# Kernel tuning notes

Hardware: AMD Instinct MI355X
Metric: run time of the kernel (lower is better)

## Reference

```python
import jax, jax.numpy as jnp
import numpy as np

SUB_NO = 20
E_NO = 2000
I_NO = 500
T_NO = 200
M_NO = 8
B_NO = 12
T_DATA = 50000


def _binary_tree_cden(sub_no):
    C = np.zeros((sub_no, sub_no), np.float32)
    for p in range(sub_no):
        for c in (2 * p + 1, 2 * p + 2):
            if c < sub_no:
                C[p, c] = 1.0
    return jnp.asarray(C)


def _syn_assign(n_syn, sub_no):
    # one-hot synapse -> subunit assignment, [sub_no, n_syn]
    return jax.nn.one_hot(jnp.arange(n_syn) % sub_no, sub_no, dtype=jnp.float32).T


def setup_inputs() -> dict:
    key = jax.random.key(0)
    ks = jax.random.split(key, 12)
    S_e = jax.random.uniform(ks[0], (T_DATA, E_NO), jnp.float32)
    S_i = jax.random.uniform(ks[1], (T_DATA, I_NO), jnp.float32)
    # parameters (scaled randn so tanh/exp stay in a sane range)
    conv1_e_bases = jax.random.normal(ks[2], (B_NO, T_NO), jnp.float32)
    conv1_e_weights = 0.001 * jax.random.normal(ks[3], (M_NO * SUB_NO, B_NO), jnp.float32)
    conv1_i_bases = jax.random.normal(ks[4], (B_NO, T_NO), jnp.float32)
    conv1_i_weights = 0.001 * jax.random.normal(ks[5], (M_NO * SUB_NO, B_NO), jnp.float32)
    conv2_bases = jax.random.normal(ks[6], (B_NO, T_NO), jnp.float32)
    conv2_weights = 0.05 * jax.random.normal(ks[7], (M_NO * SUB_NO, B_NO), jnp.float32)
    leaf_linear = 0.3 * jax.random.normal(ks[8], (SUB_NO, M_NO), jnp.float32)
    multiplex_linear = 0.3 * jax.random.normal(ks[9], (SUB_NO, M_NO), jnp.float32)
    multiplex_bias = 0.3 * jax.random.normal(ks[10], (SUB_NO,), jnp.float32)
    return {
        "S_e": S_e, "S_i": S_i,
        "C_den": _binary_tree_cden(SUB_NO),
        "C_syn_e": _syn_assign(E_NO, SUB_NO),
        "C_syn_i": _syn_assign(I_NO, SUB_NO),
        "conv1_e_bases": conv1_e_bases, "conv1_e_weights": conv1_e_weights,
        "conv1_i_bases": conv1_i_bases, "conv1_i_weights": conv1_i_weights,
        "conv2_bases": conv2_bases, "conv2_weights": conv2_weights,
        "leaf_linear": leaf_linear, "multiplex_linear": multiplex_linear,
        "multiplex_bias": multiplex_bias,
    }


def _causal_conv1d(x, w, groups):
    # x: [1, C_in, T], w: [C_out, C_in/groups, K]; left-pad K-1 -> causal
    K = w.shape[-1]
    return jax.lax.conv_general_dilated(
        x, w, window_strides=(1,), padding=[(K - 1, 0)],
        feature_group_count=groups)


def reference(S_e, S_i, C_den, C_syn_e, C_syn_i,
              conv1_e_bases, conv1_e_weights, conv1_i_bases, conv1_i_weights,
              conv2_bases, conv2_weights, leaf_linear, multiplex_linear,
              multiplex_bias):
    T = S_e.shape[0]
    sub_no, M = multiplex_linear.shape
    # route synapses to subunits: [1, sub_no, T]
    Se = (S_e @ C_syn_e.T).T[None]
    Si = (S_i @ C_syn_i.T).T[None]
    # low-rank kernels: [M*sub_no, 1, T_no]
    k1e = (conv1_e_weights @ conv1_e_bases)[:, None, :]
    k1i = (conv1_i_weights @ conv1_i_bases)[:, None, :]
    k2 = (conv2_weights @ conv2_bases)[:, None, :]
    # grouped causal conv (groups = sub_no, M outputs per group)
    e1 = _causal_conv1d(Se, k1e, sub_no)[0].T.reshape(T, sub_no, M)
    i1 = _causal_conv1d(Si, k1i, sub_no)[0].T.reshape(T, sub_no, M)
    S_conv = e1 + i1  # [T, sub_no, M]
    expL = jnp.exp(leaf_linear)      # [sub_no, M]
    expM = jnp.exp(multiplex_linear)  # [sub_no, M]
    sub_out = jnp.zeros((T, sub_no), S_e.dtype)
    # reverse order: children (larger indices) computed before parents;
    # masked matmul == torch's gather of leaf children (zeros where C_den[p]==0)
    for p in range(sub_no - 1, -1, -1):
        leaf_in = (sub_out * C_den[p][None, :]) @ expL  # [T, M]
        h = jnp.tanh(S_conv[:, p, :] + leaf_in)         # [T, M]
        c2 = _causal_conv1d(h.T[None], k2[p * M:(p + 1) * M], M)[0].T  # depthwise
        g = jnp.tanh(c2)
        sub_out = sub_out.at[:, p].set(g @ expM[p] + multiplex_bias[p])
    return sub_out[:, 0]
```

## Files before the change

kernel.cpp:

```cpp
#include <hip/hip_runtime.h>
#include <math.h>

#define T_DATA 50000
#define E_NO   2000
#define I_NO   500
#define SUBN   20
#define MN     8
#define KLEN   200
#define TILE   512
#define HALO   199
#define TW     712

__device__ __forceinline__ void conv4(float acc[4], const float4 L,
                                      const float4 H, const float4 k4) {
  const float w0 = L.x, w1 = L.y, w2 = L.z, w3 = L.w;
  const float w4 = H.x, w5 = H.y, w6 = H.z;
  acc[0] += k4.x * w3; acc[1] += k4.x * w4; acc[2] += k4.x * w5; acc[3] += k4.x * w6;
  acc[0] += k4.y * w2; acc[1] += k4.y * w3; acc[2] += k4.y * w4; acc[3] += k4.y * w5;
  acc[0] += k4.z * w1; acc[1] += k4.z * w2; acc[2] += k4.z * w3; acc[3] += k4.z * w4;
  acc[0] += k4.w * w0; acc[1] += k4.w * w1; acc[2] += k4.w * w2; acc[3] += k4.w * w3;
}

__global__ __launch_bounds__(256) void precompute_k(
    const float* __restrict__ we, const float* __restrict__ be,
    const float* __restrict__ wi, const float* __restrict__ bi,
    const float* __restrict__ w2, const float* __restrict__ b2,
    float* __restrict__ k1e, float* __restrict__ k1i, float* __restrict__ k2) {
  int idx = blockIdx.x * 256 + threadIdx.x;
  if (idx >= 160 * KLEN) return;
  int row = idx / KLEN, d = idx % KLEN;
  int col = KLEN - 1 - d;
  float se = 0.f, si = 0.f, s2 = 0.f;
#pragma unroll
  for (int b = 0; b < 12; ++b) {
    se += we[row * 12 + b] * be[b * KLEN + col];
    si += wi[row * 12 + b] * bi[b * KLEN + col];
    s2 += w2[row * 12 + b] * b2[b * KLEN + col];
  }
  k1e[idx] = se; k1i[idx] = si; k2[idx] = s2;
}

__global__ __launch_bounds__(320) void route_kernel(
    const float* __restrict__ S_e, const float* __restrict__ S_i,
    float* __restrict__ Se, float* __restrict__ Si) {
  __shared__ float lds_e[1280];
  __shared__ float lds_i[500];
  int tid = threadIdx.x;
  int t0 = blockIdx.x * 4;
  for (int tt = 0; tt < 4; ++tt) {
    int t = t0 + tt;
    const float4* rowE = (const float4*)(S_e + (size_t)t * E_NO);
    float4 a = rowE[tid];
    if (tid < 180) {
      float4 b = rowE[tid + 320];
      a.x += b.x; a.y += b.y; a.z += b.z; a.w += b.w;
    }
    ((float4*)lds_e)[tid] = a;
    if (tid < 125) {
      const float4* rowI = (const float4*)(S_i + (size_t)t * I_NO);
      ((float4*)lds_i)[tid] = rowI[tid];
    }
    __syncthreads();
    if (tid < 20) {
      float s = 0.f;
#pragma unroll
      for (int k = 0; k < 64; ++k) s += lds_e[tid + 20 * k];
      Se[tid * T_DATA + t] = s;
    } else if (tid >= 64 && tid < 84) {
      int r = tid - 64;
      float s = 0.f;
#pragma unroll
      for (int k = 0; k < 25; ++k) s += lds_i[r + 20 * k];
      Si[r * T_DATA + t] = s;
    }
    __syncthreads();
  }
}

__global__ __launch_bounds__(256) void conv1_kernel(
    const float* __restrict__ Se, const float* __restrict__ Si,
    const float* __restrict__ k1e, const float* __restrict__ k1i,
    float* __restrict__ Sconv) {
  __shared__ float xe_raw[TW + 4], xi_raw[TW + 4];
  __shared__ float ke[MN * KLEN], ki[MN * KLEN];
  float* xe = xe_raw + 4;
  float* xi = xi_raw + 4;
  int s = blockIdx.y;
  int t0 = blockIdx.x * TILE;
  int tid = threadIdx.x;

  for (int idx = tid; idx < TW; idx += 256) {
    int t = t0 - HALO + idx;
    bool ok = (t >= 0) && (t < T_DATA) && (idx < 711);
    xe[idx] = ok ? Se[s * T_DATA + t] : 0.f;
    xi[idx] = ok ? Si[s * T_DATA + t] : 0.f;
  }
  for (int idx = tid; idx < MN * KLEN; idx += 256) {
    ke[idx] = k1e[s * MN * KLEN + idx];
    ki[idx] = k1i[s * MN * KLEN + idx];
  }
  __syncthreads();

  int m = tid >> 5, g = tid & 31;
  const float* kem = ke + m * KLEN;
  const float* kim = ki + m * KLEN;
  float* outp = Sconv + ((size_t)(s * MN + m)) * T_DATA + t0;

#pragma unroll 1
  for (int i = 0; i < 4; ++i) {
    const int U = 4 * g + 128 * i;
    const int S0 = U + 196;
    float4 Le = *(const float4*)(xe + S0);
    float4 He = *(const float4*)(xe + S0 + 4);
    float4 Lx = *(const float4*)(xi + S0);
    float4 Hx = *(const float4*)(xi + S0 + 4);
    float acc[4] = {0.f, 0.f, 0.f, 0.f};
    for (int d0 = 0; d0 < KLEN; d0 += 8) {
      float4 ka = *(const float4*)(kem + d0);
      float4 kb = *(const float4*)(kim + d0);
      conv4(acc, Le, He, ka);
      conv4(acc, Lx, Hx, kb);
      float4 Ne = *(const float4*)(xe + S0 - d0 - 4);
      float4 Nx = *(const float4*)(xi + S0 - d0 - 4);
      ka = *(const float4*)(kem + d0 + 4);
      kb = *(const float4*)(kim + d0 + 4);
      conv4(acc, Ne, Le, ka);
      conv4(acc, Nx, Lx, kb);
      He = Ne; Le = *(const float4*)(xe + S0 - d0 - 8);
      Hx = Nx; Lx = *(const float4*)(xi + S0 - d0 - 8);
    }
    if (t0 + U < T_DATA)
      *(float4*)(outp + U) = make_float4(acc[0], acc[1], acc[2], acc[3]);
  }
}

struct LevelArgs {
  int node[8];
  int c1[8];
  int c2[8];
};

__global__ __launch_bounds__(256) void level_kernel(
    const float* __restrict__ Sconv, const float* __restrict__ k2r,
    const float* __restrict__ leaf_lin, const float* __restrict__ mult_lin,
    const float* __restrict__ mult_bias, float* __restrict__ sub_out,
    float* __restrict__ d_out, LevelArgs args) {
  __shared__ float hbuf_raw[4 + MN * TW];
  __shared__ float k2l[MN * KLEN];
  __shared__ float red[MN * TILE];
  float* hbuf = hbuf_raw + 4;
  int tid = threadIdx.x;
  int t0 = blockIdx.x * TILE;
  int ni = blockIdx.y;
  int p = args.node[ni], c1 = args.c1[ni], c2 = args.c2[ni];

  for (int idx = tid; idx < MN * KLEN; idx += 256)
    k2l[idx] = k2r[p * MN * KLEN + idx];

  for (int m = 0; m < MN; ++m) {
    float eL1 = (c1 >= 0) ? expf(leaf_lin[c1 * MN + m]) : 0.f;
    float eL2 = (c2 >= 0) ? expf(leaf_lin[c2 * MN + m]) : 0.f;
    const float* scp = Sconv + ((size_t)(p * MN + m)) * T_DATA;
    const float* s1 = sub_out + (size_t)((c1 >= 0) ? c1 : 0) * T_DATA;
    const float* s2 = sub_out + (size_t)((c2 >= 0) ? c2 : 0) * T_DATA;
    for (int idx = tid; idx < TW; idx += 256) {
      int t = t0 - HALO + idx;
      float v = 0.f;
      if (t >= 0 && t < T_DATA && idx < 711) {
        float x = scp[t];
        if (c1 >= 0) x += eL1 * s1[t];
        if (c2 >= 0) x += eL2 * s2[t];
        v = tanhf(x);
      }
      hbuf[m * TW + idx] = v;
    }
  }
  __syncthreads();

  int m = tid >> 5, g = tid & 31;
  const float* km = k2l + m * KLEN;
  const float* hm = hbuf + m * TW;
  float eM = expf(mult_lin[p * MN + m]);

#pragma unroll 1
  for (int i = 0; i < 4; ++i) {
    const int U = 4 * g + 128 * i;
    const int S0 = U + 196;
    float4 L = *(const float4*)(hm + S0);
    float4 H = *(const float4*)(hm + S0 + 4);
    float acc[4] = {0.f, 0.f, 0.f, 0.f};
    for (int d0 = 0; d0 < KLEN; d0 += 8) {
      float4 ka = *(const float4*)(km + d0);
      conv4(acc, L, H, ka);
      float4 N = *(const float4*)(hm + S0 - d0 - 4);
      ka = *(const float4*)(km + d0 + 4);
      conv4(acc, N, L, ka);
      H = N; L = *(const float4*)(hm + S0 - d0 - 8);
    }
    *(float4*)(red + m * TILE + U) =
        make_float4(tanhf(acc[0]) * eM, tanhf(acc[1]) * eM,
                    tanhf(acc[2]) * eM, tanhf(acc[3]) * eM);
  }
  __syncthreads();

  float bias = mult_bias[p];
  float* outp = (p == 0) ? d_out : (sub_out + (size_t)p * T_DATA);
  for (int k = 0; k < 2; ++k) {
    int tl2 = tid + k * 256;
    int t = t0 + tl2;
    if (t < T_DATA) {
      float ssum = bias;
#pragma unroll
      for (int mm = 0; mm < MN; ++mm) ssum += red[mm * TILE + tl2];
      outp[t] = ssum;
    }
  }
}

extern "C" void kernel_launch(void* const* d_in, const int* in_sizes, int n_in,
                              void* d_out, int out_size, void* d_ws, size_t ws_size,
                              hipStream_t stream) {
  const float* S_e  = (const float*)d_in[0];
  const float* S_i  = (const float*)d_in[1];
  const float* c1eb = (const float*)d_in[5];
  const float* c1ew = (const float*)d_in[6];
  const float* c1ib = (const float*)d_in[7];
  const float* c1iw = (const float*)d_in[8];
  const float* c2b  = (const float*)d_in[9];
  const float* c2w  = (const float*)d_in[10];
  const float* ll   = (const float*)d_in[11];
  const float* ml   = (const float*)d_in[12];
  const float* mb   = (const float*)d_in[13];

  float* ws    = (float*)d_ws;
  float* Se    = ws;
  float* Si    = ws + 1000000;
  float* Sconv = ws + 2000000;
  float* subo  = ws + 10000000;
  float* k1e   = ws + 11000000;
  float* k1i   = k1e + 32000;
  float* k2    = k1i + 32000;
  float* out   = (float*)d_out;

  precompute_k<<<dim3(125), 256, 0, stream>>>(c1ew, c1eb, c1iw, c1ib, c2w, c2b,
                                              k1e, k1i, k2);
  route_kernel<<<dim3(T_DATA / 4), 320, 0, stream>>>(S_e, S_i, Se, Si);

  int ntiles = (T_DATA + TILE - 1) / TILE;
  conv1_kernel<<<dim3(ntiles, SUBN), 256, 0, stream>>>(Se, Si, k1e, k1i, Sconv);

  LevelArgs L4 = {{15, 16, 17, 18, 19, 0, 0, 0},
                  {-1, -1, -1, -1, -1, 0, 0, 0},
                  {-1, -1, -1, -1, -1, 0, 0, 0}};
  LevelArgs L3 = {{7, 8, 9, 10, 11, 12, 13, 14},
                  {15, 17, 19, -1, -1, -1, -1, -1},
                  {16, 18, -1, -1, -1, -1, -1, -1}};
  LevelArgs L2 = {{3, 4, 5, 6, 0, 0, 0, 0},
                  {7, 9, 11, 13, 0, 0, 0, 0},
                  {8, 10, 12, 14, 0, 0, 0, 0}};
  LevelArgs L1 = {{1, 2, 0, 0, 0, 0, 0, 0},
                  {3, 5, 0, 0, 0, 0, 0, 0},
                  {4, 6, 0, 0, 0, 0, 0, 0}};
  LevelArgs L0 = {{0, 0, 0, 0, 0, 0, 0, 0},
                  {1, 0, 0, 0, 0, 0, 0, 0},
                  {2, 0, 0, 0, 0, 0, 0, 0}};

  level_kernel<<<dim3(ntiles, 5), 256, 0, stream>>>(Sconv, k2, ll, ml, mb, subo, out, L4);
  level_kernel<<<dim3(ntiles, 8), 256, 0, stream>>>(Sconv, k2, ll, ml, mb, subo, out, L3);
  level_kernel<<<dim3(ntiles, 4), 256, 0, stream>>>(Sconv, k2, ll, ml, mb, subo, out, L2);
  level_kernel<<<dim3(ntiles, 2), 256, 0, stream>>>(Sconv, k2, ll, ml, mb, subo, out, L1);
  level_kernel<<<dim3(ntiles, 1), 256, 0, stream>>>(Sconv, k2, ll, ml, mb, subo, out, L0);
}
```

Baseline: 1.052 ms.

## Fuse kernel precompute into routing, use fast tanh, and shrink level tiles

```diff
diff --git a/kernel.cpp b/kernel.cpp
--- a/kernel.cpp
+++ b/kernel.cpp
@@ -11,6 +11,14 @@
 #define HALO   199
 #define TW     712
 
+__device__ __forceinline__ float fast_tanh(float x) {
+  float ax = fabsf(x);
+  float e  = __expf(-2.f * ax);
+  float r  = __builtin_amdgcn_rcpf(1.f + e);
+  float t  = fmaf(-2.f * e, r, 1.f);
+  return copysignf(t, x);
+}
+
 __device__ __forceinline__ void conv4(float acc[4], const float4 L,
                                       const float4 H, const float4 k4) {
   const float w0 = L.x, w1 = L.y, w2 = L.z, w3 = L.w;
@@ -21,32 +29,36 @@
   acc[0] += k4.w * w0; acc[1] += k4.w * w1; acc[2] += k4.w * w2; acc[3] += k4.w * w3;
 }
 
-__global__ __launch_bounds__(256) void precompute_k(
+__global__ __launch_bounds__(320) void route_kernel(
+    const float* __restrict__ S_e, const float* __restrict__ S_i,
+    float* __restrict__ Se, float* __restrict__ Si,
     const float* __restrict__ we, const float* __restrict__ be,
     const float* __restrict__ wi, const float* __restrict__ bi,
     const float* __restrict__ w2, const float* __restrict__ b2,
     float* __restrict__ k1e, float* __restrict__ k1i, float* __restrict__ k2) {
-  int idx = blockIdx.x * 256 + threadIdx.x;
-  if (idx >= 160 * KLEN) return;
-  int row = idx / KLEN, d = idx % KLEN;
-  int col = KLEN - 1 - d;
-  float se = 0.f, si = 0.f, s2 = 0.f;
-#pragma unroll
-  for (int b = 0; b < 12; ++b) {
-    se += we[row * 12 + b] * be[b * KLEN + col];
-    si += wi[row * 12 + b] * bi[b * KLEN + col];
-    s2 += w2[row * 12 + b] * b2[b * KLEN + col];
-  }
-  k1e[idx] = se; k1i[idx] = si; k2[idx] = s2;
-}
-
-__global__ __launch_bounds__(320) void route_kernel(
-    const float* __restrict__ S_e, const float* __restrict__ S_i,
-    float* __restrict__ Se, float* __restrict__ Si) {
   __shared__ float lds_e[1280];
   __shared__ float lds_i[500];
   int tid = threadIdx.x;
-  int t0 = blockIdx.x * 4;
+  int bid = blockIdx.x;
+
+  if (bid >= 12500) {
+    int idx = (bid - 12500) * 320 + tid;
+    if (idx < 160 * KLEN) {
+      int row = idx / KLEN, d = idx % KLEN;
+      int col = KLEN - 1 - d;
+      float se = 0.f, si = 0.f, s2 = 0.f;
+#pragma unroll
+      for (int b = 0; b < 12; ++b) {
+        se += we[row * 12 + b] * be[b * KLEN + col];
+        si += wi[row * 12 + b] * bi[b * KLEN + col];
+        s2 += w2[row * 12 + b] * b2[b * KLEN + col];
+      }
+      k1e[idx] = se; k1i[idx] = si; k2[idx] = s2;
+    }
+    return;
+  }
+
+  int t0 = bid * 4;
   for (int tt = 0; tt < 4; ++tt) {
     int t = t0 + tt;
     const float4* rowE = (const float4*)(S_e + (size_t)t * E_NO);
@@ -140,17 +152,19 @@
   int c2[8];
 };
 
+template <int LT>
 __global__ __launch_bounds__(256) void level_kernel(
     const float* __restrict__ Sconv, const float* __restrict__ k2r,
     const float* __restrict__ leaf_lin, const float* __restrict__ mult_lin,
     const float* __restrict__ mult_bias, float* __restrict__ sub_out,
     float* __restrict__ d_out, LevelArgs args) {
-  __shared__ float hbuf_raw[4 + MN * TW];
+  const int TWL = LT + KLEN;
+  __shared__ float hbuf_raw[4 + MN * (LT + KLEN)];
   __shared__ float k2l[MN * KLEN];
-  __shared__ float red[MN * TILE];
+  __shared__ float red[MN * LT];
   float* hbuf = hbuf_raw + 4;
   int tid = threadIdx.x;
-  int t0 = blockIdx.x * TILE;
+  int t0 = blockIdx.x * LT;
   int ni = blockIdx.y;
   int p = args.node[ni], c1 = args.c1[ni], c2 = args.c2[ni];
 
@@ -158,32 +172,32 @@
     k2l[idx] = k2r[p * MN * KLEN + idx];
 
   for (int m = 0; m < MN; ++m) {
-    float eL1 = (c1 >= 0) ? expf(leaf_lin[c1 * MN + m]) : 0.f;
-    float eL2 = (c2 >= 0) ? expf(leaf_lin[c2 * MN + m]) : 0.f;
+    float eL1 = (c1 >= 0) ? __expf(leaf_lin[c1 * MN + m]) : 0.f;
+    float eL2 = (c2 >= 0) ? __expf(leaf_lin[c2 * MN + m]) : 0.f;
     const float* scp = Sconv + ((size_t)(p * MN + m)) * T_DATA;
     const float* s1 = sub_out + (size_t)((c1 >= 0) ? c1 : 0) * T_DATA;
     const float* s2 = sub_out + (size_t)((c2 >= 0) ? c2 : 0) * T_DATA;
-    for (int idx = tid; idx < TW; idx += 256) {
+    for (int idx = tid; idx < TWL; idx += 256) {
       int t = t0 - HALO + idx;
       float v = 0.f;
-      if (t >= 0 && t < T_DATA && idx < 711) {
+      if (t >= 0 && t < T_DATA && idx < TWL - 1) {
         float x = scp[t];
         if (c1 >= 0) x += eL1 * s1[t];
         if (c2 >= 0) x += eL2 * s2[t];
-        v = tanhf(x);
+        v = fast_tanh(x);
       }
-      hbuf[m * TW + idx] = v;
+      hbuf[m * TWL + idx] = v;
     }
   }
   __syncthreads();
 
   int m = tid >> 5, g = tid & 31;
   const float* km = k2l + m * KLEN;
-  const float* hm = hbuf + m * TW;
-  float eM = expf(mult_lin[p * MN + m]);
+  const float* hm = hbuf + m * TWL;
+  float eM = __expf(mult_lin[p * MN + m]);
 
 #pragma unroll 1
-  for (int i = 0; i < 4; ++i) {
+  for (int i = 0; i < LT / 128; ++i) {
     const int U = 4 * g + 128 * i;
     const int S0 = U + 196;
     float4 L = *(const float4*)(hm + S0);
@@ -197,22 +211,25 @@
       conv4(acc, N, L, ka);
       H = N; L = *(const float4*)(hm + S0 - d0 - 8);
     }
-    *(float4*)(red + m * TILE + U) =
-        make_float4(tanhf(acc[0]) * eM, tanhf(acc[1]) * eM,
-                    tanhf(acc[2]) * eM, tanhf(acc[3]) * eM);
+    *(float4*)(red + m * LT + U) =
+        make_float4(fast_tanh(acc[0]) * eM, fast_tanh(acc[1]) * eM,
+                    fast_tanh(acc[2]) * eM, fast_tanh(acc[3]) * eM);
   }
   __syncthreads();
 
   float bias = mult_bias[p];
   float* outp = (p == 0) ? d_out : (sub_out + (size_t)p * T_DATA);
-  for (int k = 0; k < 2; ++k) {
+#pragma unroll
+  for (int k = 0; k < (LT + 255) / 256; ++k) {
     int tl2 = tid + k * 256;
-    int t = t0 + tl2;
-    if (t < T_DATA) {
-      float ssum = bias;
-#pragma unroll
-      for (int mm = 0; mm < MN; ++mm) ssum += red[mm * TILE + tl2];
-      outp[t] = ssum;
+    if (tl2 < LT) {
+      int t = t0 + tl2;
+      if (t < T_DATA) {
+        float ssum = bias;
+#pragma unroll
+        for (int mm = 0; mm < MN; ++mm) ssum += red[mm * LT + tl2];
+        outp[t] = ssum;
+      }
     }
   }
 }
@@ -242,12 +259,11 @@
   float* k2    = k1i + 32000;
   float* out   = (float*)d_out;
 
-  precompute_k<<<dim3(125), 256, 0, stream>>>(c1ew, c1eb, c1iw, c1ib, c2w, c2b,
-                                              k1e, k1i, k2);
-  route_kernel<<<dim3(T_DATA / 4), 320, 0, stream>>>(S_e, S_i, Se, Si);
-
-  int ntiles = (T_DATA + TILE - 1) / TILE;
-  conv1_kernel<<<dim3(ntiles, SUBN), 256, 0, stream>>>(Se, Si, k1e, k1i, Sconv);
+  route_kernel<<<dim3(12600), 320, 0, stream>>>(S_e, S_i, Se, Si,
+                                                c1ew, c1eb, c1iw, c1ib, c2w, c2b,
+                                                k1e, k1i, k2);
+
+  conv1_kernel<<<dim3(98, SUBN), 256, 0, stream>>>(Se, Si, k1e, k1i, Sconv);
 
   LevelArgs L4 = {{15, 16, 17, 18, 19, 0, 0, 0},
                   {-1, -1, -1, -1, -1, 0, 0, 0},
@@ -265,9 +281,9 @@
                   {1, 0, 0, 0, 0, 0, 0, 0},
                   {2, 0, 0, 0, 0, 0, 0, 0}};
 
-  level_kernel<<<dim3(ntiles, 5), 256, 0, stream>>>(Sconv, k2, ll, ml, mb, subo, out, L4);
-  level_kernel<<<dim3(ntiles, 8), 256, 0, stream>>>(Sconv, k2, ll, ml, mb, subo, out, L3);
-  level_kernel<<<dim3(ntiles, 4), 256, 0, stream>>>(Sconv, k2, ll, ml, mb, subo, out, L2);
-  level_kernel<<<dim3(ntiles, 2), 256, 0, stream>>>(Sconv, k2, ll, ml, mb, subo, out, L1);
-  level_kernel<<<dim3(ntiles, 1), 256, 0, stream>>>(Sconv, k2, ll, ml, mb, subo, out, L0);
-}
+  level_kernel<256><<<dim3(196, 5), 256, 0, stream>>>(Sconv, k2, ll, ml, mb, subo, out, L4);
+  level_kernel<256><<<dim3(196, 8), 256, 0, stream>>>(Sconv, k2, ll, ml, mb, subo, out, L3);
+  level_kernel<128><<<dim3(391, 4), 256, 0, stream>>>(Sconv, k2, ll, ml, mb, subo, out, L2);
+  level_kernel<128><<<dim3(391, 2), 256, 0, stream>>>(Sconv, k2, ll, ml, mb, subo, out, L1);
+  level_kernel<128><<<dim3(391, 1), 256, 0, stream>>>(Sconv, k2, ll, ml, mb, subo, out, L0);
+}
```

After: 1.004 ms. -4.6%, faster.
